# Optimization experiments

Hardware: AMD Instinct MI355X
Metric: run time of the kernel (lower is better)

Reference implementation:

```python
import jax, jax.numpy as jnp
import numpy as np
from jax import lax

K = 16  # knn_k


def _mlp(x, W1, b1, W2, b2):
    h = jax.nn.gelu(x @ W1 + b1, approximate=False)  # torch nn.GELU default = exact
    return h @ W2 + b2


def setup_inputs() -> dict:
    key = jax.random.key(0)
    ks = jax.random.split(key, 10)
    B, N, F, H = 8, 4096, 64, 128

    def xav(k, shape):
        fan_in = shape[0]
        return (jax.random.normal(k, shape, jnp.float32) / np.sqrt(fan_in)).astype(jnp.float32)

    return {
        "coords": jax.random.normal(ks[0], (B, N, 3), jnp.float32),
        "features": jax.random.normal(ks[1], (B, N, F), jnp.float32),
        "inv_W1": xav(ks[2], (6, H)), "inv_b1": jnp.zeros((H,), jnp.float32),
        "inv_W2": xav(ks[3], (H, H)), "inv_b2": jnp.zeros((H,), jnp.float32),
        "feat_W1": xav(ks[4], (F, H)), "feat_b1": jnp.zeros((H,), jnp.float32),
        "feat_W2": xav(ks[5], (H, H)), "feat_b2": jnp.zeros((H,), jnp.float32),
        "sh_W1": xav(ks[6], (2 * H, H)), "sh_b1": jnp.zeros((H,), jnp.float32),
        "sh_W2": xav(ks[7], (H, H)), "sh_b2": jnp.zeros((H,), jnp.float32),
        "g0_W": xav(ks[8], (H, 1)), "g0_b": jnp.zeros((1,), jnp.float32),
    }


def _local_geometry(coords):
    # coords: [B,N,3]
    B, N, _ = coords.shape
    k = min(K, N - 1)
    # squared pairwise distances (monotone in euclidean dist -> same kNN indices)
    sq = jnp.sum(coords * coords, axis=-1)                    # [B,N]
    dist2 = sq[:, :, None] + sq[:, None, :] - 2.0 * jnp.einsum("bnd,bmd->bnm", coords, coords)
    dist2 = lax.stop_gradient(dist2)
    eye = jnp.eye(N, dtype=bool)
    dist2 = jnp.where(eye[None], jnp.inf, dist2)
    _, idx = lax.top_k(-dist2, k)                             # smallest-k -> [B,N,k]
    neighbors = jax.vmap(lambda c, i: c[i])(coords, idx)      # [B,N,k,3]
    relative = neighbors - coords[:, :, None, :]              # [B,N,k,3]
    cov = jnp.einsum("bnki,bnkj->bnij", relative, relative) / float(k)  # [B,N,3,3]
    evals, evecs = jnp.linalg.eigh(cov)                       # ascending
    normals = evecs[..., 0]                                   # smallest-eigval eigenvector, [B,N,3]
    center = coords.mean(axis=1, keepdims=True)
    outward = coords - center
    orient = jnp.sign(jnp.sum(normals * outward, axis=-1, keepdims=True))
    orient = jnp.where(orient == 0, 1.0, orient)
    normals = normals * orient
    normals = normals / jnp.maximum(jnp.linalg.norm(normals, axis=-1, keepdims=True), 1e-6)
    radius = jnp.linalg.norm(relative, axis=-1).mean(axis=-1, keepdims=True)   # [B,N,1]
    centered_radius = jnp.linalg.norm(outward, axis=-1, keepdims=True)
    eig_sum = jnp.maximum(evals.sum(axis=-1, keepdims=True), 1e-6)
    dominance = evals[..., 2:3] / eig_sum
    invariants = jnp.concatenate([evals, radius, centered_radius, dominance], axis=-1)  # [B,N,6]
    return normals, invariants


def reference(coords, features, inv_W1, inv_b1, inv_W2, inv_b2,
              feat_W1, feat_b1, feat_W2, feat_b2,
              sh_W1, sh_b1, sh_W2, sh_b2, g0_W, g0_b):
    normals, invariants = _local_geometry(coords)
    inv_h = _mlp(invariants, inv_W1, inv_b1, inv_W2, inv_b2)
    feat_h = _mlp(features, feat_W1, feat_b1, feat_W2, feat_b2)
    hidden = _mlp(jnp.concatenate([inv_h, feat_h], axis=-1), sh_W1, sh_b1, sh_W2, sh_b2)
    scalar = hidden @ g0_W + g0_b                                   # grade 0, [B,N,1]
    plane = jnp.stack([normals[..., 0], normals[..., 1], -normals[..., 2],
                       -jnp.sum(coords * normals, axis=-1)], axis=-1)  # grade 1, [B,N,4]
    biv = jnp.concatenate([normals, jnp.zeros_like(normals)], axis=-1)  # grade 2, [B,N,6]
    point = jnp.concatenate([coords, jnp.ones(coords.shape[:-1] + (1,), coords.dtype)], axis=-1)  # grade 3 OPNS point
    zero4 = jnp.zeros(coords.shape[:-1] + (1,), coords.dtype)            # grade 4
    return jnp.concatenate([scalar, plane, biv, point, zero4], axis=-1)  # [B,N,16]
```

## Files before the change

### kernel.cpp

```cpp
#include <hip/hip_runtime.h>
#include <hip/hip_bf16.h>

#define BB 8
#define NN 4096
#define FF 64
#define HH 128
#define KNN 16

typedef __attribute__((ext_vector_type(8))) short bf16x8;
typedef __attribute__((ext_vector_type(4))) float f32x4;

#define OFF_iW2 0
#define OFF_fW1 16384
#define OFF_fW2 24576
#define OFF_sW1 40960
#define OFF_sW2 73728
#define HI_SZ   90112

__device__ __forceinline__ float sq3(float x, float y, float z) {
    return fmaf(z, z, fmaf(y, y, __fmul_rn(x, x)));
}
__device__ __forceinline__ float dist2f(float px, float py, float pz, float psq, float4 cc) {
    float t = fmaf(pz, cc.z, fmaf(py, cc.y, __fmul_rn(px, cc.x)));
    return __fsub_rn(__fadd_rn(psq, cc.w), __fmul_rn(2.0f, t));
}

__device__ __forceinline__ short f2bf(float x) {
    unsigned u = __float_as_uint(x);
    u += 0x7fffu + ((u >> 16) & 1u);
    return (short)(u >> 16);
}
__device__ __forceinline__ float bf2f(short s) {
    return __uint_as_float(((unsigned)(unsigned short)s) << 16);
}

extern "C" __global__ __launch_bounds__(256)
void k_prep(const float* __restrict__ coords, float4* __restrict__ coords4, float* __restrict__ center) {
    const int b = blockIdx.x, tid = threadIdx.x;
    __shared__ float rx[256], ry[256], rz[256];
    float sx = 0.f, sy = 0.f, sz = 0.f;
    for (int n = tid; n < NN; n += 256) {
        const float* c = coords + (size_t)(b * NN + n) * 3;
        float x = c[0], y = c[1], z = c[2];
        coords4[b * NN + n] = make_float4(x, y, z, sq3(x, y, z));
        sx += x; sy += y; sz += z;
    }
    rx[tid] = sx; ry[tid] = sy; rz[tid] = sz;
    __syncthreads();
    for (int s = 128; s > 0; s >>= 1) {
        if (tid < s) { rx[tid] += rx[tid + s]; ry[tid] += ry[tid + s]; rz[tid] += rz[tid + s]; }
        __syncthreads();
    }
    if (tid == 0) {
        center[b * 4 + 0] = rx[0] * (1.0f / NN);
        center[b * 4 + 1] = ry[0] * (1.0f / NN);
        center[b * 4 + 2] = rz[0] * (1.0f / NN);
    }
}

extern "C" __global__ __launch_bounds__(256)
void k_wprep(const float* __restrict__ iW2, const float* __restrict__ fW1,
             const float* __restrict__ fW2, const float* __restrict__ sW1,
             const float* __restrict__ sW2, short* __restrict__ wbf) {
    const int w = blockIdx.y;
    const float* W; int K; int off;
    if (w == 0)      { W = iW2; K = 128; off = OFF_iW2; }
    else if (w == 1) { W = fW1; K = 64;  off = OFF_fW1; }
    else if (w == 2) { W = fW2; K = 128; off = OFF_fW2; }
    else if (w == 3) { W = sW1; K = 256; off = OFF_sW1; }
    else             { W = sW2; K = 128; off = OFF_sW2; }
    short* hi = wbf + off;
    short* lo = wbf + HI_SZ + off;
    const int total = K * 128;
    for (int e = blockIdx.x * 256 + threadIdx.x; e < total; e += gridDim.x * 256) {
        int j = e & 7, lane = (e >> 3) & 63, ct = (e >> 9) & 7, kb = e >> 12;
        int k = kb * 32 + (lane >> 4) * 8 + j;
        int n = ct * 16 + (lane & 15);
        float v = W[k * 128 + n];
        short h = f2bf(v);
        float r = v - bf2f(h);
        hi[e] = h; lo[e] = f2bf(r);
    }
}

#define JROT(app, aqq, apq, arp, arq, vp0, vp1, vp2, vq0, vq1, vq2) { \
    float tau_ = (aqq - app) / (2.0f * apq); \
    float tt_ = copysignf(1.0f, tau_) / (fabsf(tau_) + sqrtf(1.0f + tau_ * tau_)); \
    if (apq == 0.0f) tt_ = 0.0f; \
    float cc_ = 1.0f / sqrtf(1.0f + tt_ * tt_); \
    float ss_ = tt_ * cc_; \
    float app_n = cc_*cc_*app - 2.0f*cc_*ss_*apq + ss_*ss_*aqq; \
    float aqq_n = ss_*ss_*app + 2.0f*cc_*ss_*apq + cc_*cc_*aqq; \
    float apq_n = cc_*ss_*(app - aqq) + (cc_*cc_ - ss_*ss_)*apq; \
    float arp_n = cc_*arp - ss_*arq; \
    float arq_n = ss_*arp + cc_*arq; \
    app = app_n; aqq = aqq_n; apq = apq_n; arp = arp_n; arq = arq_n; \
    float t0_ = cc_*vp0 - ss_*vq0, t1_ = cc_*vp1 - ss_*vq1, t2_ = cc_*vp2 - ss_*vq2; \
    vq0 = ss_*vp0 + cc_*vq0; vq1 = ss_*vp1 + cc_*vq1; vq2 = ss_*vp2 + cc_*vq2; \
    vp0 = t0_; vp1 = t1_; vp2 = t2_; }

#define SWAPF(a, b) { float sw_ = a; a = b; b = sw_; }

__device__ __forceinline__ void sort16(float (&d)[16]) {
#pragma unroll
    for (int k = 2; k <= 16; k <<= 1) {
#pragma unroll
        for (int j = k >> 1; j > 0; j >>= 1) {
#pragma unroll
            for (int i = 0; i < 16; i++) {
                int l = i ^ j;
                if (l > i) {
                    if ((i & k) == 0) {
                        float mn = fminf(d[i], d[l]);
                        d[l] = fmaxf(d[i], d[l]);
                        d[i] = mn;
                    } else {
                        float mx = fmaxf(d[i], d[l]);
                        d[l] = fminf(d[i], d[l]);
                        d[i] = mx;
                    }
                }
            }
        }
    }
}

__device__ __forceinline__ void merge16(float (&dk)[16], const float (&d)[16]) {
    float t[16];
#pragma unroll
    for (int i = 0; i < 16; i++) t[i] = fminf(dk[i], d[15 - i]);
#pragma unroll
    for (int j = 8; j > 0; j >>= 1) {
#pragma unroll
        for (int i = 0; i < 16; i++) {
            int l = i ^ j;
            if (l > i) {
                float mn = fminf(t[i], t[l]);
                t[l] = fmaxf(t[i], t[l]);
                t[i] = mn;
            }
        }
    }
#pragma unroll
    for (int i = 0; i < 16; i++) dk[i] = t[i];
}

__device__ __forceinline__ float gelu_exact(float x) {
    return 0.5f * x * (1.0f + erff(x * 0.70710678118654752440f));
}

template <int KDIM, int LDA>
__device__ __forceinline__ void gemm_small(const float* A, const float* __restrict__ W,
                                           const float* __restrict__ bias, int p0, int c0, float acc[4][4]) {
    float4 bb = *(const float4*)(bias + c0);
#pragma unroll
    for (int i = 0; i < 4; i++) { acc[i][0] = bb.x; acc[i][1] = bb.y; acc[i][2] = bb.z; acc[i][3] = bb.w; }
#pragma unroll
    for (int k = 0; k < KDIM; k++) {
        float4 w = *(const float4*)(W + k * HH + c0);
#pragma unroll
        for (int i = 0; i < 4; i++) {
            float a = A[(p0 + i) * LDA + k];
            acc[i][0] = fmaf(a, w.x, acc[i][0]);
            acc[i][1] = fmaf(a, w.y, acc[i][1]);
            acc[i][2] = fmaf(a, w.z, acc[i][2]);
            acc[i][3] = fmaf(a, w.w, acc[i][3]);
        }
    }
}

template <int KB, bool INIT>
__device__ __forceinline__ void gemm_mfma(const short* Ab, const short* __restrict__ whi,
                                          const short* __restrict__ wlo,
                                          const float* __restrict__ bias,
                                          int wid, int lane, f32x4 acc[2][2]) {
    const int m16 = lane & 15, quad = lane >> 4;
    if (INIT) {
        float b0 = bias[(wid * 2 + 0) * 16 + m16];
        float b1 = bias[(wid * 2 + 1) * 16 + m16];
        acc[0][0] = (f32x4){b0, b0, b0, b0}; acc[1][0] = acc[0][0];
        acc[0][1] = (f32x4){b1, b1, b1, b1}; acc[1][1] = acc[0][1];
    }
#pragma unroll 1
    for (int kb = 0; kb < KB; kb++) {
        bf16x8 a0 = *(const bf16x8*)(Ab + m16 * 136 + kb * 32 + quad * 8);
        bf16x8 a1 = *(const bf16x8*)(Ab + (m16 + 16) * 136 + kb * 32 + quad * 8);
#pragma unroll
        for (int c = 0; c < 2; c++) {
            const int off = ((kb * 8 + wid * 2 + c) * 64 + lane) * 8;
            bf16x8 bh = *(const bf16x8*)(whi + off);
            bf16x8 bl = *(const bf16x8*)(wlo + off);
            acc[0][c] = __builtin_amdgcn_mfma_f32_16x16x32_bf16(a0, bh, acc[0][c], 0, 0, 0);
            acc[0][c] = __builtin_amdgcn_mfma_f32_16x16x32_bf16(a0, bl, acc[0][c], 0, 0, 0);
            acc[1][c] = __builtin_amdgcn_mfma_f32_16x16x32_bf16(a1, bh, acc[1][c], 0, 0, 0);
            acc[1][c] = __builtin_amdgcn_mfma_f32_16x16x32_bf16(a1, bl, acc[1][c], 0, 0, 0);
        }
    }
}

__device__ __forceinline__ void acc_to_stage(float* fstage, f32x4 acc[2][2], int wid, int lane, bool dogelu) {
    const int m16 = lane & 15, quad = lane >> 4;
#pragma unroll
    for (int mt = 0; mt < 2; mt++)
#pragma unroll
        for (int c = 0; c < 2; c++)
#pragma unroll
            for (int i = 0; i < 4; i++) {
                float v = acc[mt][c][i];
                if (dogelu) v = gelu_exact(v);
                fstage[(mt * 16 + quad * 4 + i) * 128 + (wid * 2 + c) * 16 + m16] = v;
            }
}

__device__ __forceinline__ void cvt_stage(const float* fstage, short* dst, int tid) {
#pragma unroll
    for (int it = 0; it < 2; it++) {
        int idx = tid + it * 256;
        int row = idx >> 4, c8 = (idx & 15) * 8;
        const float* s = fstage + row * 128 + c8;
        float4 v0 = *(const float4*)s, v1 = *(const float4*)(s + 4);
        bf16x8 pk;
        pk[0] = f2bf(v0.x); pk[1] = f2bf(v0.y); pk[2] = f2bf(v0.z); pk[3] = f2bf(v0.w);
        pk[4] = f2bf(v1.x); pk[5] = f2bf(v1.y); pk[6] = f2bf(v1.z); pk[7] = f2bf(v1.w);
        *(bf16x8*)(dst + row * 136 + c8) = pk;
    }
}

__device__ __forceinline__ void store4f(float* dst, float a, float b, float c, float d) {
    *(float4*)dst = make_float4(a, b, c, d);
}

extern "C" __global__ __launch_bounds__(256, 4)
void k_fused(const float4* __restrict__ coords4, const float* __restrict__ center,
             const float* __restrict__ features, const short* __restrict__ wbf,
             const float* __restrict__ iW1, const float* __restrict__ ib1,
             const float* __restrict__ ib2,
             const float* __restrict__ fb1, const float* __restrict__ fb2,
             const float* __restrict__ sb1, const float* __restrict__ sb2,
             const float* __restrict__ gW, const float* __restrict__ gb,
             float* __restrict__ out) {
    const int blk = blockIdx.x;
    const int b = blk >> 7;
    const int chunk = blk & 127;
    const int tid = threadIdx.x;
    const int pid = tid & 31;
    const int h = tid >> 5;
    const int n = chunk * 32 + pid;
    const float4* __restrict__ C = coords4 + b * NN;

    __shared__ __align__(16) char smem[34944];
    float4* tile = (float4*)smem;
    int* ilist = (int*)(smem + 8192);
    int* cnts = (int*)(smem + 32768);
    float* inv8 = (float*)(smem + 33792);
    float* sc = (float*)(smem + 34816);
    float* mb = (float*)ilist;
    float* fstage = (float*)smem;
    short* Abf = (short*)(smem + 16384);
    short* FHbf = (short*)(smem + 25088);

    float4 me = C[n];
    const float px = me.x, py = me.y, pz = me.z, psq = me.w;
    const float INF = __builtin_inff();

    float dk[KNN];
#pragma unroll
    for (int i = 0; i < KNN; i++) dk[i] = INF;

    for (int r = 0; r < 8; r++) {
        __syncthreads();
#pragma unroll
        for (int e = tid; e < 512; e += 256) {
            int seg = e >> 6, idx = e & 63;
            tile[e] = C[seg * 512 + r * 64 + idx];
        }
        __syncthreads();
        const float4* T = &tile[h * 64];
        const int selfj = n - (h * 512 + r * 64);
#pragma unroll
        for (int bt = 0; bt < 4; bt++) {
            float d[16];
#pragma unroll
            for (int i = 0; i < 16; i++) {
                float4 cc = T[bt * 16 + i];
                float dd = dist2f(px, py, pz, psq, cc);
                d[i] = (bt * 16 + i) == selfj ? INF : dd;
            }
            sort16(d);
            merge16(dk, d);
        }
    }

    __syncthreads();
#pragma unroll
    for (int i = 0; i < KNN; i++) mb[tid * 17 + i] = dk[i];
    __syncthreads();
#pragma unroll
    for (int p = 1; p < 8; p++) {
        const int partner = (((h + p) & 7) << 5) + pid;
        float o[16];
#pragma unroll
        for (int i = 0; i < KNN; i++) o[i] = mb[partner * 17 + i];
        merge16(dk, o);
    }
    const float d15 = dk[15];

    int cs = 0, ct = 0;
    const int lbase = (pid * 8 + h) * 24;
    for (int r = 0; r < 8; r++) {
        __syncthreads();
#pragma unroll
        for (int e = tid; e < 512; e += 256) {
            int seg = e >> 6, idx = e & 63;
            tile[e] = C[seg * 512 + r * 64 + idx];
        }
        __syncthreads();
        const float4* T = &tile[h * 64];
        const int base = h * 512 + r * 64;
#pragma unroll 4
        for (int j = 0; j < 64; j++) {
            float4 cc = T[j];
            float d = dist2f(px, py, pz, psq, cc);
            int g = base + j;
            if (g != n && d <= d15) {
                if (d < d15) {
                    if (cs < 15) ilist[lbase + cs] = g;
                    cs++;
                } else if (ct < 8) {
                    ilist[lbase + 15 + ct] = g;
                    ct++;
                }
            }
        }
    }
    cnts[pid * 8 + h] = (cs & 0xff) | (ct << 8);
    __syncthreads();

    if (h == 0) {
        int s[8], t8[8], sb[8], tb[8], cum[8], tcum[8];
#pragma unroll
        for (int q = 0; q < 8; q++) {
            int cp = cnts[pid * 8 + q];
            s[q] = cp & 0xff; t8[q] = cp >> 8;
            sb[q] = (pid * 8 + q) * 24; tb[q] = sb[q] + 15;
        }
        cum[0] = s[0]; tcum[0] = t8[0];
#pragma unroll
        for (int q = 1; q < 8; q++) { cum[q] = cum[q - 1] + s[q]; tcum[q] = tcum[q - 1] + t8[q]; }

        float cxx = 0.f, cxy = 0.f, cxz = 0.f, cyy = 0.f, cyz = 0.f, czz = 0.f, radsum = 0.f;
#pragma unroll
        for (int j = 0; j < KNN; j++) {
            int addr = sb[0] + j;
#pragma unroll
            for (int q = 1; q < 8; q++)
                if (j >= cum[q - 1]) addr = sb[q] + (j - cum[q - 1]);
            int jt = j - cum[7];
            if (j >= cum[7]) addr = tb[0] + jt;
#pragma unroll
            for (int q = 1; q < 8; q++)
                if (j >= cum[7] && jt >= tcum[q - 1]) addr = tb[q] + (jt - tcum[q - 1]);
            int id = ilist[addr];
            float4 cc = C[id];
            float rx = __fsub_rn(cc.x, px), ry = __fsub_rn(cc.y, py), rz = __fsub_rn(cc.z, pz);
            cxx = __fadd_rn(cxx, __fmul_rn(rx, rx));
            cxy = __fadd_rn(cxy, __fmul_rn(rx, ry));
            cxz = __fadd_rn(cxz, __fmul_rn(rx, rz));
            cyy = __fadd_rn(cyy, __fmul_rn(ry, ry));
            cyz = __fadd_rn(cyz, __fmul_rn(ry, rz));
            czz = __fadd_rn(czz, __fmul_rn(rz, rz));
            float rr = __fadd_rn(__fadd_rn(__fmul_rn(rx, rx), __fmul_rn(ry, ry)), __fmul_rn(rz, rz));
            radsum = __fadd_rn(radsum, sqrtf(rr));
        }
        const float inv_k = 1.0f / KNN;
        float a00 = cxx * inv_k, a01 = cxy * inv_k, a02 = cxz * inv_k;
        float a11 = cyy * inv_k, a12 = cyz * inv_k, a22 = czz * inv_k;

        float V00 = 1.f, V01 = 0.f, V02 = 0.f;
        float V10 = 0.f, V11 = 1.f, V12 = 0.f;
        float V20 = 0.f, V21 = 0.f, V22 = 1.f;
        for (int sweep = 0; sweep < 6; sweep++) {
            JROT(a00, a11, a01, a02, a12, V00, V10, V20, V01, V11, V21);
            JROT(a00, a22, a02, a01, a12, V00, V10, V20, V02, V12, V22);
            JROT(a11, a22, a12, a01, a02, V01, V11, V21, V02, V12, V22);
        }
        float e0 = a00, e1 = a11, e2 = a22;
        float x0 = V00, y0 = V10, z0 = V20;
        float x1 = V01, y1 = V11, z1 = V21;
        float x2 = V02, y2 = V12, z2 = V22;
        if (e0 > e1) { SWAPF(e0, e1); SWAPF(x0, x1); SWAPF(y0, y1); SWAPF(z0, z1); }
        if (e1 > e2) { SWAPF(e1, e2); SWAPF(x1, x2); SWAPF(y1, y2); SWAPF(z1, z2); }
        if (e0 > e1) { SWAPF(e0, e1); SWAPF(x0, x1); SWAPF(y0, y1); SWAPF(z0, z1); }

        float cx = center[b * 4 + 0], cy = center[b * 4 + 1], cz = center[b * 4 + 2];
        float ox = __fsub_rn(px, cx), oy = __fsub_rn(py, cy), oz = __fsub_rn(pz, cz);
        float dt = __fadd_rn(__fadd_rn(__fmul_rn(x0, ox), __fmul_rn(y0, oy)), __fmul_rn(z0, oz));
        float sgn = (dt >= 0.0f) ? 1.0f : -1.0f;
        x0 *= sgn; y0 *= sgn; z0 *= sgn;
        float nrm = sqrtf(__fadd_rn(__fadd_rn(__fmul_rn(x0, x0), __fmul_rn(y0, y0)), __fmul_rn(z0, z0)));
        float den = fmaxf(nrm, 1e-6f);
        x0 = x0 / den; y0 = y0 / den; z0 = z0 / den;

        float radius = radsum * inv_k;
        float crad = sqrtf(__fadd_rn(__fadd_rn(__fmul_rn(ox, ox), __fmul_rn(oy, oy)), __fmul_rn(oz, oz)));
        float esum = fmaxf(__fadd_rn(__fadd_rn(e0, e1), e2), 1e-6f);
        float dom = e2 / esum;

        float* ip = inv8 + pid * 8;
        ip[0] = e0; ip[1] = e1; ip[2] = e2; ip[3] = radius; ip[4] = crad; ip[5] = dom;
        ip[6] = 0.f; ip[7] = 0.f;

        float pd = __fadd_rn(__fadd_rn(__fmul_rn(px, x0), __fmul_rn(py, y0)), __fmul_rn(pz, z0));
        float4* o = (float4*)(out + (size_t)(b * NN + n) * 16);
        o[0] = make_float4(0.0f, x0, y0, -z0);
        o[1] = make_float4(-pd, x0, y0, z0);
        o[2] = make_float4(0.0f, 0.0f, 0.0f, px);
        o[3] = make_float4(py, pz, 1.0f, 0.0f);
        sc[pid] = gb[0];
    }
    __syncthreads();

    const int wid = tid >> 6, lane = tid & 63;
    const short* w_iW2h = wbf + OFF_iW2; const short* w_iW2l = wbf + HI_SZ + OFF_iW2;
    const short* w_fW1h = wbf + OFF_fW1; const short* w_fW1l = wbf + HI_SZ + OFF_fW1;
    const short* w_fW2h = wbf + OFF_fW2; const short* w_fW2l = wbf + HI_SZ + OFF_fW2;
    const short* w_sW1h = wbf + OFF_sW1; const short* w_sW1l = wbf + HI_SZ + OFF_sW1;
    const short* w_sW2h = wbf + OFF_sW2; const short* w_sW2l = wbf + HI_SZ + OFF_sW2;
    f32x4 acc[2][2];

    {
        int row = tid >> 3, c8 = (tid & 7) * 8;
        const float* s = features + (size_t)(b * NN + chunk * 32 + row) * FF + c8;
        float4 v0 = *(const float4*)s, v1 = *(const float4*)(s + 4);
        bf16x8 pk;
        pk[0] = f2bf(v0.x); pk[1] = f2bf(v0.y); pk[2] = f2bf(v0.z); pk[3] = f2bf(v0.w);
        pk[4] = f2bf(v1.x); pk[5] = f2bf(v1.y); pk[6] = f2bf(v1.z); pk[7] = f2bf(v1.w);
        *(bf16x8*)(Abf + row * 136 + c8) = pk;
    }
    __syncthreads();

    gemm_mfma<2, true>(Abf, w_fW1h, w_fW1l, fb1, wid, lane, acc);
    acc_to_stage(fstage, acc, wid, lane, true);
    __syncthreads();
    cvt_stage(fstage, Abf, tid);
    __syncthreads();

    gemm_mfma<4, true>(Abf, w_fW2h, w_fW2l, fb2, wid, lane, acc);
    acc_to_stage(fstage, acc, wid, lane, false);
    __syncthreads();
    cvt_stage(fstage, FHbf, tid);
    __syncthreads();

    {
        const int cg = tid & 31, pg = tid >> 5;
        const int c0 = cg * 4, p0 = pg * 4;
        float a4[4][4];
        gemm_small<6, 8>(inv8, iW1, ib1, p0, c0, a4);
#pragma unroll
        for (int i = 0; i < 4; i++)
            store4f(&fstage[(p0 + i) * 128 + c0], gelu_exact(a4[i][0]), gelu_exact(a4[i][1]),
                    gelu_exact(a4[i][2]), gelu_exact(a4[i][3]));
    }
    __syncthreads();
    cvt_stage(fstage, Abf, tid);
    __syncthreads();

    gemm_mfma<4, true>(Abf, w_iW2h, w_iW2l, ib2, wid, lane, acc);
    acc_to_stage(fstage, acc, wid, lane, false);
    __syncthreads();
    cvt_stage(fstage, Abf, tid);
    __syncthreads();

    gemm_mfma<4, true>(Abf, w_sW1h, w_sW1l, sb1, wid, lane, acc);
    gemm_mfma<4, false>(FHbf, w_sW1h + 16384, w_sW1l + 16384, nullptr, wid, lane, acc);
    acc_to_stage(fstage, acc, wid, lane, true);
    __syncthreads();
    cvt_stage(fstage, Abf, tid);
    __syncthreads();

    gemm_mfma<4, true>(Abf, w_sW2h, w_sW2l, sb2, wid, lane, acc);
    {
        const int m16 = lane & 15, quad = lane >> 4;
#pragma unroll
        for (int mt = 0; mt < 2; mt++)
#pragma unroll
            for (int c = 0; c < 2; c++) {
                float g = gW[(wid * 2 + c) * 16 + m16];
#pragma unroll
                for (int i = 0; i < 4; i++)
                    atomicAdd(&sc[mt * 16 + quad * 4 + i], acc[mt][c][i] * g);
            }
    }
    __syncthreads();
    if (tid < 32) out[(size_t)(b * NN + n) * 16] = sc[tid];
}

extern "C" void kernel_launch(void* const* d_in, const int* in_sizes, int n_in,
                              void* d_out, int out_size, void* d_ws, size_t ws_size,
                              hipStream_t stream) {
    const float* coords   = (const float*)d_in[0];
    const float* features = (const float*)d_in[1];
    const float* iW1 = (const float*)d_in[2],  * ib1 = (const float*)d_in[3];
    const float* iW2 = (const float*)d_in[4],  * ib2 = (const float*)d_in[5];
    const float* fW1 = (const float*)d_in[6],  * fb1 = (const float*)d_in[7];
    const float* fW2 = (const float*)d_in[8],  * fb2 = (const float*)d_in[9];
    const float* sW1 = (const float*)d_in[10], * sb1 = (const float*)d_in[11];
    const float* sW2 = (const float*)d_in[12], * sb2 = (const float*)d_in[13];
    const float* gW  = (const float*)d_in[14], * gb  = (const float*)d_in[15];
    float* out = (float*)d_out;

    float* ws = (float*)d_ws;
    float4* coords4 = (float4*)ws;
    float* center = ws + BB * NN * 4;
    short* wbf = (short*)((char*)d_ws + 524416);

    hipLaunchKernelGGL(k_prep, dim3(BB), dim3(256), 0, stream, coords, coords4, center);
    hipLaunchKernelGGL(k_wprep, dim3(16, 5), dim3(256), 0, stream, iW2, fW1, fW2, sW1, sW2, wbf);
    hipLaunchKernelGGL(k_fused, dim3(1024), dim3(256), 0, stream, coords4, center, features, wbf,
                       iW1, ib1, ib2, fb1, fb2, sb1, sb2, gW, gb, out);
}
```

Before: 286.7 us.

## Double fused-kernel block to 512 threads, merge prep kernels, stage MLP activations directly in bf16

Measured after the change: 265.7 us. 7.3% less time.

```diff
diff --git a/kernel.cpp b/kernel.cpp
--- a/kernel.cpp
+++ b/kernel.cpp
@@ -8,6 +8,7 @@
 #define KNN 16
 
 typedef __attribute__((ext_vector_type(8))) short bf16x8;
+typedef __attribute__((ext_vector_type(4))) short bf16x4;
 typedef __attribute__((ext_vector_type(4))) float f32x4;
 
 #define OFF_iW2 0
@@ -35,51 +36,54 @@
 }
 
 extern "C" __global__ __launch_bounds__(256)
-void k_prep(const float* __restrict__ coords, float4* __restrict__ coords4, float* __restrict__ center) {
-    const int b = blockIdx.x, tid = threadIdx.x;
+void k_prep(const float* __restrict__ coords, float4* __restrict__ coords4, float* __restrict__ center,
+            const float* __restrict__ iW2, const float* __restrict__ fW1,
+            const float* __restrict__ fW2, const float* __restrict__ sW1,
+            const float* __restrict__ sW2, short* __restrict__ wbf) {
+    const int bx = blockIdx.x, tid = threadIdx.x;
     __shared__ float rx[256], ry[256], rz[256];
-    float sx = 0.f, sy = 0.f, sz = 0.f;
-    for (int n = tid; n < NN; n += 256) {
-        const float* c = coords + (size_t)(b * NN + n) * 3;
-        float x = c[0], y = c[1], z = c[2];
-        coords4[b * NN + n] = make_float4(x, y, z, sq3(x, y, z));
-        sx += x; sy += y; sz += z;
-    }
-    rx[tid] = sx; ry[tid] = sy; rz[tid] = sz;
-    __syncthreads();
-    for (int s = 128; s > 0; s >>= 1) {
-        if (tid < s) { rx[tid] += rx[tid + s]; ry[tid] += ry[tid + s]; rz[tid] += rz[tid + s]; }
-        __syncthreads();
-    }
-    if (tid == 0) {
-        center[b * 4 + 0] = rx[0] * (1.0f / NN);
-        center[b * 4 + 1] = ry[0] * (1.0f / NN);
-        center[b * 4 + 2] = rz[0] * (1.0f / NN);
-    }
-}
-
-extern "C" __global__ __launch_bounds__(256)
-void k_wprep(const float* __restrict__ iW2, const float* __restrict__ fW1,
-             const float* __restrict__ fW2, const float* __restrict__ sW1,
-             const float* __restrict__ sW2, short* __restrict__ wbf) {
-    const int w = blockIdx.y;
-    const float* W; int K; int off;
-    if (w == 0)      { W = iW2; K = 128; off = OFF_iW2; }
-    else if (w == 1) { W = fW1; K = 64;  off = OFF_fW1; }
-    else if (w == 2) { W = fW2; K = 128; off = OFF_fW2; }
-    else if (w == 3) { W = sW1; K = 256; off = OFF_sW1; }
-    else             { W = sW2; K = 128; off = OFF_sW2; }
-    short* hi = wbf + off;
-    short* lo = wbf + HI_SZ + off;
-    const int total = K * 128;
-    for (int e = blockIdx.x * 256 + threadIdx.x; e < total; e += gridDim.x * 256) {
-        int j = e & 7, lane = (e >> 3) & 63, ct = (e >> 9) & 7, kb = e >> 12;
-        int k = kb * 32 + (lane >> 4) * 8 + j;
-        int n = ct * 16 + (lane & 15);
-        float v = W[k * 128 + n];
-        short h = f2bf(v);
-        float r = v - bf2f(h);
-        hi[e] = h; lo[e] = f2bf(r);
+    if (bx < 8) {
+        const int b = bx;
+        float sx = 0.f, sy = 0.f, sz = 0.f;
+        for (int n = tid; n < NN; n += 256) {
+            const float* c = coords + (size_t)(b * NN + n) * 3;
+            float x = c[0], y = c[1], z = c[2];
+            coords4[b * NN + n] = make_float4(x, y, z, sq3(x, y, z));
+            sx += x; sy += y; sz += z;
+        }
+        rx[tid] = sx; ry[tid] = sy; rz[tid] = sz;
+        __syncthreads();
+        for (int s = 128; s > 0; s >>= 1) {
+            if (tid < s) { rx[tid] += rx[tid + s]; ry[tid] += ry[tid + s]; rz[tid] += rz[tid + s]; }
+            __syncthreads();
+        }
+        if (tid == 0) {
+            center[b * 4 + 0] = rx[0] * (1.0f / NN);
+            center[b * 4 + 1] = ry[0] * (1.0f / NN);
+            center[b * 4 + 2] = rz[0] * (1.0f / NN);
+        }
+    } else {
+        const int wb = bx - 8;
+        const int w = wb >> 4;
+        const int xb = wb & 15;
+        const float* W; int K; int off;
+        if (w == 0)      { W = iW2; K = 128; off = OFF_iW2; }
+        else if (w == 1) { W = fW1; K = 64;  off = OFF_fW1; }
+        else if (w == 2) { W = fW2; K = 128; off = OFF_fW2; }
+        else if (w == 3) { W = sW1; K = 256; off = OFF_sW1; }
+        else             { W = sW2; K = 128; off = OFF_sW2; }
+        short* hi = wbf + off;
+        short* lo = wbf + HI_SZ + off;
+        const int total = K * 128;
+        for (int e = xb * 256 + tid; e < total; e += 4096) {
+            int j = e & 7, lane = (e >> 3) & 63, ct = (e >> 9) & 7, kb = e >> 12;
+            int k = kb * 32 + (lane >> 4) * 8 + j;
+            int n = ct * 16 + (lane & 15);
+            float v = W[k * 128 + n];
+            short h = f2bf(v);
+            float r = v - bf2f(h);
+            hi[e] = h; lo[e] = f2bf(r);
+        }
     }
 }
 
@@ -145,92 +149,68 @@
     for (int i = 0; i < 16; i++) dk[i] = t[i];
 }
 
+__device__ __forceinline__ void sort16i(int (&d)[16]) {
+#pragma unroll
+    for (int k = 2; k <= 16; k <<= 1) {
+#pragma unroll
+        for (int j = k >> 1; j > 0; j >>= 1) {
+#pragma unroll
+            for (int i = 0; i < 16; i++) {
+                int l = i ^ j;
+                if (l > i) {
+                    int a = d[i], bq = d[l];
+                    int mn = a < bq ? a : bq;
+                    int mx = a < bq ? bq : a;
+                    if ((i & k) == 0) { d[i] = mn; d[l] = mx; }
+                    else              { d[i] = mx; d[l] = mn; }
+                }
+            }
+        }
+    }
+}
+
 __device__ __forceinline__ float gelu_exact(float x) {
     return 0.5f * x * (1.0f + erff(x * 0.70710678118654752440f));
-}
-
-template <int KDIM, int LDA>
-__device__ __forceinline__ void gemm_small(const float* A, const float* __restrict__ W,
-                                           const float* __restrict__ bias, int p0, int c0, float acc[4][4]) {
-    float4 bb = *(const float4*)(bias + c0);
-#pragma unroll
-    for (int i = 0; i < 4; i++) { acc[i][0] = bb.x; acc[i][1] = bb.y; acc[i][2] = bb.z; acc[i][3] = bb.w; }
-#pragma unroll
-    for (int k = 0; k < KDIM; k++) {
-        float4 w = *(const float4*)(W + k * HH + c0);
-#pragma unroll
-        for (int i = 0; i < 4; i++) {
-            float a = A[(p0 + i) * LDA + k];
-            acc[i][0] = fmaf(a, w.x, acc[i][0]);
-            acc[i][1] = fmaf(a, w.y, acc[i][1]);
-            acc[i][2] = fmaf(a, w.z, acc[i][2]);
-            acc[i][3] = fmaf(a, w.w, acc[i][3]);
-        }
-    }
 }
 
 template <int KB, bool INIT>
 __device__ __forceinline__ void gemm_mfma(const short* Ab, const short* __restrict__ whi,
                                           const short* __restrict__ wlo,
                                           const float* __restrict__ bias,
-                                          int wid, int lane, f32x4 acc[2][2]) {
+                                          int wid, int lane, f32x4 acc[2]) {
     const int m16 = lane & 15, quad = lane >> 4;
     if (INIT) {
-        float b0 = bias[(wid * 2 + 0) * 16 + m16];
-        float b1 = bias[(wid * 2 + 1) * 16 + m16];
-        acc[0][0] = (f32x4){b0, b0, b0, b0}; acc[1][0] = acc[0][0];
-        acc[0][1] = (f32x4){b1, b1, b1, b1}; acc[1][1] = acc[0][1];
+        float b0 = bias[wid * 16 + m16];
+        acc[0] = (f32x4){b0, b0, b0, b0};
+        acc[1] = acc[0];
     }
 #pragma unroll 1
     for (int kb = 0; kb < KB; kb++) {
         bf16x8 a0 = *(const bf16x8*)(Ab + m16 * 136 + kb * 32 + quad * 8);
         bf16x8 a1 = *(const bf16x8*)(Ab + (m16 + 16) * 136 + kb * 32 + quad * 8);
-#pragma unroll
-        for (int c = 0; c < 2; c++) {
-            const int off = ((kb * 8 + wid * 2 + c) * 64 + lane) * 8;
-            bf16x8 bh = *(const bf16x8*)(whi + off);
-            bf16x8 bl = *(const bf16x8*)(wlo + off);
-            acc[0][c] = __builtin_amdgcn_mfma_f32_16x16x32_bf16(a0, bh, acc[0][c], 0, 0, 0);
-            acc[0][c] = __builtin_amdgcn_mfma_f32_16x16x32_bf16(a0, bl, acc[0][c], 0, 0, 0);
-            acc[1][c] = __builtin_amdgcn_mfma_f32_16x16x32_bf16(a1, bh, acc[1][c], 0, 0, 0);
-            acc[1][c] = __builtin_amdgcn_mfma_f32_16x16x32_bf16(a1, bl, acc[1][c], 0, 0, 0);
-        }
-    }
-}
-
-__device__ __forceinline__ void acc_to_stage(float* fstage, f32x4 acc[2][2], int wid, int lane, bool dogelu) {
+        const int off = ((kb * 8 + wid) * 64 + lane) * 8;
+        bf16x8 bh = *(const bf16x8*)(whi + off);
+        bf16x8 bl = *(const bf16x8*)(wlo + off);
+        acc[0] = __builtin_amdgcn_mfma_f32_16x16x32_bf16(a0, bh, acc[0], 0, 0, 0);
+        acc[0] = __builtin_amdgcn_mfma_f32_16x16x32_bf16(a0, bl, acc[0], 0, 0, 0);
+        acc[1] = __builtin_amdgcn_mfma_f32_16x16x32_bf16(a1, bh, acc[1], 0, 0, 0);
+        acc[1] = __builtin_amdgcn_mfma_f32_16x16x32_bf16(a1, bl, acc[1], 0, 0, 0);
+    }
+}
+
+__device__ __forceinline__ void acc_to_bf(short* dst, f32x4 acc[2], int wid, int lane, bool dogelu) {
     const int m16 = lane & 15, quad = lane >> 4;
 #pragma unroll
     for (int mt = 0; mt < 2; mt++)
 #pragma unroll
-        for (int c = 0; c < 2; c++)
-#pragma unroll
-            for (int i = 0; i < 4; i++) {
-                float v = acc[mt][c][i];
-                if (dogelu) v = gelu_exact(v);
-                fstage[(mt * 16 + quad * 4 + i) * 128 + (wid * 2 + c) * 16 + m16] = v;
-            }
-}
-
-__device__ __forceinline__ void cvt_stage(const float* fstage, short* dst, int tid) {
-#pragma unroll
-    for (int it = 0; it < 2; it++) {
-        int idx = tid + it * 256;
-        int row = idx >> 4, c8 = (idx & 15) * 8;
-        const float* s = fstage + row * 128 + c8;
-        float4 v0 = *(const float4*)s, v1 = *(const float4*)(s + 4);
-        bf16x8 pk;
-        pk[0] = f2bf(v0.x); pk[1] = f2bf(v0.y); pk[2] = f2bf(v0.z); pk[3] = f2bf(v0.w);
-        pk[4] = f2bf(v1.x); pk[5] = f2bf(v1.y); pk[6] = f2bf(v1.z); pk[7] = f2bf(v1.w);
-        *(bf16x8*)(dst + row * 136 + c8) = pk;
-    }
-}
-
-__device__ __forceinline__ void store4f(float* dst, float a, float b, float c, float d) {
-    *(float4*)dst = make_float4(a, b, c, d);
-}
-
-extern "C" __global__ __launch_bounds__(256, 4)
+        for (int i = 0; i < 4; i++) {
+            float v = acc[mt][i];
+            if (dogelu) v = gelu_exact(v);
+            dst[(mt * 16 + quad * 4 + i) * 136 + wid * 16 + m16] = f2bf(v);
+        }
+}
+
+extern "C" __global__ __launch_bounds__(512, 8)
 void k_fused(const float4* __restrict__ coords4, const float* __restrict__ center,
              const float* __restrict__ features, const short* __restrict__ wbf,
              const float* __restrict__ iW1, const float* __restrict__ ib1,
@@ -248,16 +228,17 @@
     const int n = chunk * 32 + pid;
     const float4* __restrict__ C = coords4 + b * NN;
 
-    __shared__ __align__(16) char smem[34944];
+    __shared__ __align__(16) char smem[36864];
     float4* tile = (float4*)smem;
-    int* ilist = (int*)(smem + 8192);
-    int* cnts = (int*)(smem + 32768);
-    float* inv8 = (float*)(smem + 33792);
-    float* sc = (float*)(smem + 34816);
-    float* mb = (float*)ilist;
-    float* fstage = (float*)smem;
-    short* Abf = (short*)(smem + 16384);
-    short* FHbf = (short*)(smem + 25088);
+    float* mb = (float*)smem;
+    unsigned short* slist = (unsigned short*)(smem + 16384);
+    unsigned short* tlist = (unsigned short*)(smem + 17408);
+    int* cnt_s = (int*)(smem + 17920);
+    int* cnt_t = (int*)(smem + 18048);
+    float* inv8 = (float*)(smem + 18176);
+    float* sc   = (float*)(smem + 19200);
+    short* Abf  = (short*)(smem + 19328);
+    short* FHbf = (short*)(smem + 28032);
 
     float4 me = C[n];
     const float px = me.x, py = me.y, pz = me.z, psq = me.w;
@@ -267,16 +248,16 @@
 #pragma unroll
     for (int i = 0; i < KNN; i++) dk[i] = INF;
 
-    for (int r = 0; r < 8; r++) {
-        __syncthreads();
-#pragma unroll
-        for (int e = tid; e < 512; e += 256) {
+    for (int r = 0; r < 4; r++) {
+        __syncthreads();
+#pragma unroll
+        for (int e = tid; e < 1024; e += 512) {
             int seg = e >> 6, idx = e & 63;
-            tile[e] = C[seg * 512 + r * 64 + idx];
+            tile[e] = C[seg * 256 + r * 64 + idx];
         }
         __syncthreads();
         const float4* T = &tile[h * 64];
-        const int selfj = n - (h * 512 + r * 64);
+        const int selfj = n - (h * 256 + r * 64);
 #pragma unroll
         for (int bt = 0; bt < 4; bt++) {
             float d[16];
@@ -291,32 +272,39 @@
         }
     }
 
-    __syncthreads();
-#pragma unroll
-    for (int i = 0; i < KNN; i++) mb[tid * 17 + i] = dk[i];
-    __syncthreads();
-#pragma unroll
-    for (int p = 1; p < 8; p++) {
-        const int partner = (((h + p) & 7) << 5) + pid;
+    {
         float o[16];
 #pragma unroll
-        for (int i = 0; i < KNN; i++) o[i] = mb[partner * 17 + i];
+        for (int i = 0; i < KNN; i++) o[i] = __shfl_xor(dk[i], 32);
         merge16(dk, o);
     }
+#pragma unroll
+    for (int s = 64; s <= 256; s <<= 1) {
+        __syncthreads();
+#pragma unroll
+        for (int i = 0; i < KNN; i++) mb[tid * 17 + i] = dk[i];
+        __syncthreads();
+        const int ptn = tid ^ s;
+        float o[16];
+#pragma unroll
+        for (int i = 0; i < KNN; i++) o[i] = mb[ptn * 17 + i];
+        merge16(dk, o);
+    }
     const float d15 = dk[15];
 
-    int cs = 0, ct = 0;
-    const int lbase = (pid * 8 + h) * 24;
-    for (int r = 0; r < 8; r++) {
-        __syncthreads();
-#pragma unroll
-        for (int e = tid; e < 512; e += 256) {
+    __syncthreads();
+    if (tid < 32) { cnt_s[tid] = 0; cnt_t[tid] = 0; }
+
+    for (int r = 0; r < 4; r++) {
+        __syncthreads();
+#pragma unroll
+        for (int e = tid; e < 1024; e += 512) {
             int seg = e >> 6, idx = e & 63;
-            tile[e] = C[seg * 512 + r * 64 + idx];
+            tile[e] = C[seg * 256 + r * 64 + idx];
         }
         __syncthreads();
         const float4* T = &tile[h * 64];
-        const int base = h * 512 + r * 64;
+        const int base = h * 256 + r * 64;
 #pragma unroll 4
         for (int j = 0; j < 64; j++) {
             float4 cc = T[j];
@@ -324,44 +312,33 @@
             int g = base + j;
             if (g != n && d <= d15) {
                 if (d < d15) {
-                    if (cs < 15) ilist[lbase + cs] = g;
-                    cs++;
-                } else if (ct < 8) {
-                    ilist[lbase + 15 + ct] = g;
-                    ct++;
+                    int pos = atomicAdd(&cnt_s[pid], 1);
+                    if (pos < 16) slist[pid * 16 + pos] = (unsigned short)g;
+                } else {
+                    int pos = atomicAdd(&cnt_t[pid], 1);
+                    if (pos < 8) tlist[pid * 8 + pos] = (unsigned short)g;
                 }
             }
         }
     }
-    cnts[pid * 8 + h] = (cs & 0xff) | (ct << 8);
-    __syncthreads();
-
-    if (h == 0) {
-        int s[8], t8[8], sb[8], tb[8], cum[8], tcum[8];
-#pragma unroll
-        for (int q = 0; q < 8; q++) {
-            int cp = cnts[pid * 8 + q];
-            s[q] = cp & 0xff; t8[q] = cp >> 8;
-            sb[q] = (pid * 8 + q) * 24; tb[q] = sb[q] + 15;
-        }
-        cum[0] = s[0]; tcum[0] = t8[0];
-#pragma unroll
-        for (int q = 1; q < 8; q++) { cum[q] = cum[q - 1] + s[q]; tcum[q] = tcum[q - 1] + t8[q]; }
+    __syncthreads();
+
+    if (tid < 32) {
+        int ns = cnt_s[tid]; ns = ns > 15 ? 15 : ns;
+        int ids[16];
+#pragma unroll
+        for (int j = 0; j < 16; j++) {
+            int tj = j - ns; tj = tj < 0 ? 0 : (tj > 7 ? 7 : tj);
+            int sid = (int)slist[tid * 16 + j];
+            int tie = (int)tlist[tid * 8 + tj];
+            ids[j] = (j < ns) ? sid : tie;
+        }
+        sort16i(ids);
 
         float cxx = 0.f, cxy = 0.f, cxz = 0.f, cyy = 0.f, cyz = 0.f, czz = 0.f, radsum = 0.f;
 #pragma unroll
         for (int j = 0; j < KNN; j++) {
-            int addr = sb[0] + j;
-#pragma unroll
-            for (int q = 1; q < 8; q++)
-                if (j >= cum[q - 1]) addr = sb[q] + (j - cum[q - 1]);
-            int jt = j - cum[7];
-            if (j >= cum[7]) addr = tb[0] + jt;
-#pragma unroll
-            for (int q = 1; q < 8; q++)
-                if (j >= cum[7] && jt >= tcum[q - 1]) addr = tb[q] + (jt - tcum[q - 1]);
-            int id = ilist[addr];
-            float4 cc = C[id];
+            float4 cc = C[ids[j]];
             float rx = __fsub_rn(cc.x, px), ry = __fsub_rn(cc.y, py), rz = __fsub_rn(cc.z, pz);
             cxx = __fadd_rn(cxx, __fmul_rn(rx, rx));
             cxy = __fadd_rn(cxy, __fmul_rn(rx, ry));
@@ -406,7 +383,7 @@
         float esum = fmaxf(__fadd_rn(__fadd_rn(e0, e1), e2), 1e-6f);
         float dom = e2 / esum;
 
-        float* ip = inv8 + pid * 8;
+        float* ip = inv8 + tid * 8;
         ip[0] = e0; ip[1] = e1; ip[2] = e2; ip[3] = radius; ip[4] = crad; ip[5] = dom;
         ip[6] = 0.f; ip[7] = 0.f;
 
@@ -416,7 +393,7 @@
         o[1] = make_float4(-pd, x0, y0, z0);
         o[2] = make_float4(0.0f, 0.0f, 0.0f, px);
         o[3] = make_float4(py, pz, 1.0f, 0.0f);
-        sc[pid] = gb[0];
+        sc[tid] = gb[0];
     }
     __syncthreads();
 
@@ -426,73 +403,79 @@
     const short* w_fW2h = wbf + OFF_fW2; const short* w_fW2l = wbf + HI_SZ + OFF_fW2;
     const short* w_sW1h = wbf + OFF_sW1; const short* w_sW1l = wbf + HI_SZ + OFF_sW1;
     const short* w_sW2h = wbf + OFF_sW2; const short* w_sW2l = wbf + HI_SZ + OFF_sW2;
-    f32x4 acc[2][2];
+    f32x4 acc[2];
 
     {
-        int row = tid >> 3, c8 = (tid & 7) * 8;
-        const float* s = features + (size_t)(b * NN + chunk * 32 + row) * FF + c8;
-        float4 v0 = *(const float4*)s, v1 = *(const float4*)(s + 4);
-        bf16x8 pk;
-        pk[0] = f2bf(v0.x); pk[1] = f2bf(v0.y); pk[2] = f2bf(v0.z); pk[3] = f2bf(v0.w);
-        pk[4] = f2bf(v1.x); pk[5] = f2bf(v1.y); pk[6] = f2bf(v1.z); pk[7] = f2bf(v1.w);
-        *(bf16x8*)(Abf + row * 136 + c8) = pk;
+        int row = tid >> 4, c4 = (tid & 15) * 4;
+        const float* s = features + (size_t)(b * NN + chunk * 32 + row) * FF + c4;
+        float4 v = *(const float4*)s;
+        bf16x4 pk;
+        pk[0] = f2bf(v.x); pk[1] = f2bf(v.y); pk[2] = f2bf(v.z); pk[3] = f2bf(v.w);
+        *(bf16x4*)(Abf + row * 136 + c4) = pk;
     }
     __syncthreads();
 
     gemm_mfma<2, true>(Abf, w_fW1h, w_fW1l, fb1, wid, lane, acc);
-    acc_to_stage(fstage, acc, wid, lane, true);
-    __syncthreads();
-    cvt_stage(fstage, Abf, tid);
+    __syncthreads();
+    acc_to_bf(Abf, acc, wid, lane, true);
     __syncthreads();
 
     gemm_mfma<4, true>(Abf, w_fW2h, w_fW2l, fb2, wid, lane, acc);
-    acc_to_stage(fstage, acc, wid, lane, false);
-    __syncthreads();
-    cvt_stage(fstage, FHbf, tid);
-    __syncthreads();
+    __syncthreads();
+    acc_to_bf(FHbf, acc, wid, lane, false);
 
     {
         const int cg = tid & 31, pg = tid >> 5;
-        const int c0 = cg * 4, p0 = pg * 4;
-        float a4[4][4];
-        gemm_small<6, 8>(inv8, iW1, ib1, p0, c0, a4);
-#pragma unroll
-        for (int i = 0; i < 4; i++)
-            store4f(&fstage[(p0 + i) * 128 + c0], gelu_exact(a4[i][0]), gelu_exact(a4[i][1]),
-                    gelu_exact(a4[i][2]), gelu_exact(a4[i][3]));
-    }
-    __syncthreads();
-    cvt_stage(fstage, Abf, tid);
+        const int c0 = cg * 4, p0 = pg * 2;
+        float4 bb = *(const float4*)(ib1 + c0);
+        float a2[2][4];
+#pragma unroll
+        for (int i = 0; i < 2; i++) { a2[i][0] = bb.x; a2[i][1] = bb.y; a2[i][2] = bb.z; a2[i][3] = bb.w; }
+#pragma unroll
+        for (int k = 0; k < 6; k++) {
+            float4 w = *(const float4*)(iW1 + k * HH + c0);
+#pragma unroll
+            for (int i = 0; i < 2; i++) {
+                float a = inv8[(p0 + i) * 8 + k];
+                a2[i][0] = fmaf(a, w.x, a2[i][0]);
+                a2[i][1] = fmaf(a, w.y, a2[i][1]);
+                a2[i][2] = fmaf(a, w.z, a2[i][2]);
+                a2[i][3] = fmaf(a, w.w, a2[i][3]);
+            }
+        }
+#pragma unroll
+        for (int i = 0; i < 2; i++) {
+            bf16x4 pk;
+            pk[0] = f2bf(gelu_exact(a2[i][0])); pk[1] = f2bf(gelu_exact(a2[i][1]));
+            pk[2] = f2bf(gelu_exact(a2[i][2])); pk[3] = f2bf(gelu_exact(a2[i][3]));
+            *(bf16x4*)(Abf + (p0 + i) * 136 + c0) = pk;
+        }
+    }
     __syncthreads();
 
     gemm_mfma<4, true>(Abf, w_iW2h, w_iW2l, ib2, wid, lane, acc);
-    acc_to_stage(fstage, acc, wid, lane, false);
-    __syncthreads();
-    cvt_stage(fstage, Abf, tid);
+    __syncthreads();
+    acc_to_bf(Abf, acc, wid, lane, false);
     __syncthreads();
 
     gemm_mfma<4, true>(Abf, w_sW1h, w_sW1l, sb1, wid, lane, acc);
     gemm_mfma<4, false>(FHbf, w_sW1h + 16384, w_sW1l + 16384, nullptr, wid, lane, acc);
-    acc_to_stage(fstage, acc, wid, lane, true);
-    __syncthreads();
-    cvt_stage(fstage, Abf, tid);
+    __syncthreads();
+    acc_to_bf(Abf, acc, wid, lane, true);
     __syncthreads();
 
     gemm_mfma<4, true>(Abf, w_sW2h, w_sW2l, sb2, wid, lane, acc);
     {
         const int m16 = lane & 15, quad = lane >> 4;
+        float g = gW[wid * 16 + m16];
 #pragma unroll
         for (int mt = 0; mt < 2; mt++)
 #pragma unroll
-            for (int c = 0; c < 2; c++) {
-                float g = gW[(wid * 2 + c) * 16 + m16];
-#pragma unroll
-                for (int i = 0; i < 4; i++)
-                    atomicAdd(&sc[mt * 16 + quad * 4 + i], acc[mt][c][i] * g);
-            }
-    }
-    __syncthreads();
-    if (tid < 32) out[(size_t)(b * NN + n) * 16] = sc[tid];
+            for (int i = 0; i < 4; i++)
+                atomicAdd(&sc[mt * 16 + quad * 4 + i], acc[mt][i] * g);
+    }
+    __syncthreads();
+    if (tid < 32) out[(size_t)(b * NN + chunk * 32 + tid) * 16] = sc[tid];
 }
 
 extern "C" void kernel_launch(void* const* d_in, const int* in_sizes, int n_in,
@@ -514,8 +497,8 @@
     float* center = ws + BB * NN * 4;
     short* wbf = (short*)((char*)d_ws + 524416);
 
-    hipLaunchKernelGGL(k_prep, dim3(BB), dim3(256), 0, stream, coords, coords4, center);
-    hipLaunchKernelGGL(k_wprep, dim3(16, 5), dim3(256), 0, stream, iW2, fW1, fW2, sW1, sW2, wbf);
-    hipLaunchKernelGGL(k_fused, dim3(1024), dim3(256), 0, stream, coords4, center, features, wbf,
+    hipLaunchKernelGGL(k_prep, dim3(88), dim3(256), 0, stream,
+                       coords, coords4, center, iW2, fW1, fW2, sW1, sW2, wbf);
+    hipLaunchKernelGGL(k_fused, dim3(1024), dim3(512), 0, stream, coords4, center, features, wbf,
                        iW1, ib1, ib2, fb1, fb2, sb1, sb2, gW, gb, out);
 }
```
